# Kernel optimization log

Hardware: AMD Instinct MI355X
Metric: run time of the kernel (lower is better)

## Reference

```python
import jax, jax.numpy as jnp
import numpy as np

N = 100000   # input nodes
M = 100000   # output nodes (size = (N, M))
NNZ = 3_200_000  # edges, avg_degree 32
B = 32       # batch
D = 32       # Kaiming channel dim


def setup_inputs() -> dict:
    key = jax.random.key(0)
    k1, k2, k3 = jax.random.split(key, 3)
    # COO indices: row 0 = src (in [0, N)), row 1 = dst (in [0, M))
    indices = jax.random.randint(k1, (2, NNZ), 0, N, dtype=jnp.int32)
    # Kaiming init: randn * sqrt(2/d), as in the torch module when d is given
    values = jax.random.normal(k2, (NNZ,), dtype=jnp.float32) * np.float32((2.0 / D) ** 0.5)
    bias = jnp.zeros((M, 1), dtype=jnp.float32)
    x = jax.random.normal(k3, (B, N, 1), dtype=jnp.float32)
    return {"x": x, "indices": indices, "values": values, "bias": bias}


def reference(x, indices, values, bias):
    # Equivalent of: for each b, sparse.mm(W.T, x[b]) + bias, W in COO (N, M)
    # y[b, m] = sum_{e: dst[e]==m} values[e] * x[b, src[e]] + bias[m]
    src = indices[0]
    dst = indices[1]
    contrib = x[:, src, 0] * values[None, :]           # (B, NNZ) gather-multiply
    y = jax.ops.segment_sum(contrib.T, dst, num_segments=M)  # (M, B) scatter-add
    return (y.T + bias[:, 0][None, :])[..., None]       # (B, M, 1)
```

## Files before the change

### kernel.cpp

```cpp
#include <hip/hip_runtime.h>
#include <hip/hip_fp16.h>
#include <stdint.h>

#define NB 32
#define CSHIFT 7
#define CROWS 128
#define NC_MAX 1024
#define FCHUNK 8192
#define FTHREADS 1024
#define EPT (FCHUNK / FTHREADS)
#define CAP_C 4608
#define GTHREADS 512
#define NGW 8
#define GEPT ((CAP_C + GTHREADS - 1) / GTHREADS)
#define SRC_BITS 18
#define SRC_MASK ((1u << SRC_BITS) - 1)


__global__ void transpose_x_kernel(const float* __restrict__ x,
                                   __half* __restrict__ xt,
                                   int* __restrict__ zeroRegion, int N) {
    __shared__ float tile[32][33];
    if (blockIdx.x == 0) {
        int i = threadIdx.y * 32 + threadIdx.x;
        for (; i < NC_MAX + 4; i += 256) zeroRegion[i] = 0;
    }
    int n0 = blockIdx.x * 32;
    for (int i = threadIdx.y; i < 32; i += 8) {
        int n = n0 + threadIdx.x;
        tile[i][threadIdx.x] = (n < N) ? x[(size_t)i * N + n] : 0.f;
    }
    __syncthreads();
    for (int i = threadIdx.y; i < 32; i += 8) {
        int n = n0 + i;
        if (n < N) xt[(size_t)n * NB + threadIdx.x] =
            __float2half(tile[threadIdx.x][i]);
    }
}

__global__ __launch_bounds__(1024) void fill_coarse(
        const int* __restrict__ src,
        const int* __restrict__ dst,
        const float* __restrict__ vals,
        int* __restrict__ cCursor,
        uint2* __restrict__ csr,
        int* __restrict__ ovCount,
        int* __restrict__ ovList,
        int nnz) {
    __shared__ uint2 stage[FCHUNK];
    __shared__ unsigned short binOf[FCHUNK];
    __shared__ int lhist[NC_MAX];
    __shared__ int lbase[NC_MAX];
    __shared__ int delta[NC_MAX];
    int t = threadIdx.x;
    int e0 = blockIdx.x * FCHUNK;
    int chunk = min(FCHUNK, nnz - e0);
    int dcache[EPT], scache[EPT];
    float vcache[EPT];
    lhist[t] = 0;
    __syncthreads();
#pragma unroll
    for (int q = 0; q < EPT; ++q) {
        int e = e0 + q * FTHREADS + t;
        if (e < nnz) {
            int d = dst[e];
            dcache[q] = d;
            scache[q] = src[e];
            vcache[q] = vals[e];
            atomicAdd(&lhist[d >> CSHIFT], 1);
        } else dcache[q] = -1;
    }
    __syncthreads();
    int v = lhist[t];
    lbase[t] = v;
    __syncthreads();
    for (int off = 1; off < NC_MAX; off <<= 1) {
        int add = (t >= off) ? lbase[t - off] : 0;
        __syncthreads();
        lbase[t] += add;
        __syncthreads();
    }
    {
        int excl = lbase[t] - v;
        lbase[t] = excl;
        int grel = v ? atomicAdd(&cCursor[t], v) : 0;
        delta[t] = grel - excl;
        lhist[t] = 0;
    }
    __syncthreads();
#pragma unroll
    for (int q = 0; q < EPT; ++q) {
        int d = dcache[q];
        if (d >= 0) {
            int bin = d >> CSHIFT;
            int r = atomicAdd(&lhist[bin], 1);
            int pos = lbase[bin] + r;
            if (delta[bin] + pos < CAP_C) {
                stage[pos] = make_uint2(
                    ((uint32_t)(d & (CROWS - 1)) << SRC_BITS) |
                        (uint32_t)scache[q],
                    __float_as_uint(vcache[q]));
                binOf[pos] = (unsigned short)bin;
            } else {
                binOf[pos] = 0xFFFF;
                int op = atomicAdd(ovCount, 1);
                ovList[op] = e0 + q * FTHREADS + t;
            }
        }
    }
    __syncthreads();
    for (int idx = t; idx < chunk; idx += FTHREADS) {
        unsigned short bo = binOf[idx];
        if (bo != 0xFFFF)
            csr[(size_t)bo * CAP_C + delta[bo] + idx] = stage[idx];
    }
}

__global__ __launch_bounds__(GTHREADS) void region_sort_gather(
        const int* __restrict__ cCursor,
        const uint2* __restrict__ cCsr,
        const __half* __restrict__ xt,
        const float* __restrict__ bias,
        float* __restrict__ out, int M) {
    __shared__ uint2 sorted[CAP_C];
    __shared__ int whist[NGW][CROWS];
    __shared__ int rowOff[CROWS];
    __shared__ int rowCnt[CROWS];
    int c = blockIdx.x;
    int n = min(cCursor[c], CAP_C);
    int t = threadIdx.x;
    int w = t >> 6;
    uint2 ec[GEPT];
    for (int i = t; i < NGW * CROWS; i += GTHREADS) (&whist[0][0])[i] = 0;
    __syncthreads();
    const uint2* reg = cCsr + (size_t)c * CAP_C;
#pragma unroll
    for (int q = 0; q < GEPT; ++q) {
        int j = q * GTHREADS + t;
        if (j < n) {
            uint2 e = reg[j];
            ec[q] = e;
            atomicAdd(&whist[w][(e.x >> SRC_BITS) & (CROWS - 1)], 1);
        }
    }
    __syncthreads();
    int tot = 0;
    if (t < CROWS) {
#pragma unroll
        for (int w2 = 0; w2 < NGW; ++w2) tot += whist[w2][t];
        rowCnt[t] = tot;
        rowOff[t] = tot;
    }
    __syncthreads();
    for (int off = 1; off < CROWS; off <<= 1) {
        int add = (t < CROWS && t >= off) ? rowOff[t - off] : 0;
        __syncthreads();
        if (t < CROWS) rowOff[t] += add;
        __syncthreads();
    }
    if (t < CROWS) {
        int excl = rowOff[t] - rowCnt[t];
        rowOff[t] = excl;
        int run = excl;
#pragma unroll
        for (int w2 = 0; w2 < NGW; ++w2) {
            int cn = whist[w2][t];
            whist[w2][t] = run;
            run += cn;
        }
    }
    __syncthreads();
#pragma unroll
    for (int q = 0; q < GEPT; ++q) {
        int j = q * GTHREADS + t;
        if (j < n) {
            uint2 e = ec[q];
            int p = atomicAdd(&whist[w][(e.x >> SRC_BITS) & (CROWS - 1)], 1);
            sorted[p] = e;
        }
    }
    __syncthreads();
    int g = t >> 5;
    int b = t & 31;
    for (int r = g; r < CROWS; r += GTHREADS / 32) {
        int m = c * CROWS + r;
        if (m >= M) break;
        int jj   = rowOff[r];
        int jend = jj + rowCnt[r];
        float acc0 = 0.f, acc1 = 0.f;
        for (; jj + 8 <= jend; jj += 8) {
            uint2 e0 = sorted[jj + 0];
            uint2 e1 = sorted[jj + 1];
            uint2 e2 = sorted[jj + 2];
            uint2 e3 = sorted[jj + 3];
            uint2 e4 = sorted[jj + 4];
            uint2 e5 = sorted[jj + 5];
            uint2 e6 = sorted[jj + 6];
            uint2 e7 = sorted[jj + 7];
            float x0 = __half2float(xt[(size_t)(e0.x & SRC_MASK) * NB + b]);
            float x1 = __half2float(xt[(size_t)(e1.x & SRC_MASK) * NB + b]);
            float x2 = __half2float(xt[(size_t)(e2.x & SRC_MASK) * NB + b]);
            float x3 = __half2float(xt[(size_t)(e3.x & SRC_MASK) * NB + b]);
            float x4 = __half2float(xt[(size_t)(e4.x & SRC_MASK) * NB + b]);
            float x5 = __half2float(xt[(size_t)(e5.x & SRC_MASK) * NB + b]);
            float x6 = __half2float(xt[(size_t)(e6.x & SRC_MASK) * NB + b]);
            float x7 = __half2float(xt[(size_t)(e7.x & SRC_MASK) * NB + b]);
            acc0 = fmaf(__uint_as_float(e0.y), x0, acc0);
            acc1 = fmaf(__uint_as_float(e1.y), x1, acc1);
            acc0 = fmaf(__uint_as_float(e2.y), x2, acc0);
            acc1 = fmaf(__uint_as_float(e3.y), x3, acc1);
            acc0 = fmaf(__uint_as_float(e4.y), x4, acc0);
            acc1 = fmaf(__uint_as_float(e5.y), x5, acc1);
            acc0 = fmaf(__uint_as_float(e6.y), x6, acc0);
            acc1 = fmaf(__uint_as_float(e7.y), x7, acc1);
        }
        for (; jj < jend; ++jj) {
            uint2 e = sorted[jj];
            acc0 = fmaf(__uint_as_float(e.y),
                        __half2float(xt[(size_t)(e.x & SRC_MASK) * NB + b]),
                        acc0);
        }
        out[(size_t)b * M + m] = acc0 + acc1 + bias[m];
    }
}

__global__ void fixup_kernel(const int* __restrict__ ovCount,
                             const int* __restrict__ ovList,
                             const int* __restrict__ src,
                             const int* __restrict__ dst,
                             const float* __restrict__ vals,
                             const __half* __restrict__ xt,
                             float* __restrict__ out, int M) {
    long long total = (long long)(*ovCount) * 32;
    long long stride = (long long)gridDim.x * blockDim.x;
    for (long long i = (long long)blockIdx.x * blockDim.x + threadIdx.x;
         i < total; i += stride) {
        int k = (int)(i >> 5);
        int b = (int)(i & 31);
        int e = ovList[k];
        atomicAdd(&out[(size_t)b * M + dst[e]],
                  vals[e] * __half2float(xt[(size_t)src[e] * NB + b]));
    }
}

__global__ void finalize_kernel(const float* __restrict__ yt,
                                const float* __restrict__ bias,
                                float* __restrict__ out, int M) {
    __shared__ float tile[32][33];
    int m0 = blockIdx.x * 32;
    for (int i = threadIdx.y; i < 32; i += 8) {
        int m = m0 + i;
        tile[i][threadIdx.x] = (m < M) ? yt[(size_t)m * NB + threadIdx.x] : 0.f;
    }
    __syncthreads();
    for (int i = threadIdx.y; i < 32; i += 8) {
        int m = m0 + threadIdx.x;
        if (m < M) out[(size_t)i * M + m] = tile[threadIdx.x][i] + bias[m];
    }
}

__global__ void scatter_kernel(const int* __restrict__ src,
                               const int* __restrict__ dst,
                               const float* __restrict__ vals,
                               const __half* __restrict__ xt,
                               float* __restrict__ yt, int nnz) {
    long long tid = (long long)blockIdx.x * blockDim.x + threadIdx.x;
    int e = (int)(tid >> 5);
    if (e >= nnz) return;
    int b = (int)(tid & 31);
    atomicAdd(&yt[(size_t)dst[e] * NB + b],
              vals[e] * __half2float(xt[(size_t)src[e] * NB + b]));
}

extern "C" void kernel_launch(void* const* d_in, const int* in_sizes, int n_in,
                              void* d_out, int out_size, void* d_ws, size_t ws_size,
                              hipStream_t stream) {
    const float* x       = (const float*)d_in[0];
    const int*   indices = (const int*)  d_in[1];
    const float* vals    = (const float*)d_in[2];
    const float* bias    = (const float*)d_in[3];

    float* out = (float*)d_out;

    int nnz = in_sizes[1] / 2;
    int N   = in_sizes[0] / NB;
    int M   = in_sizes[3];

    const int* src = indices;
    const int* dst = indices + nnz;

    int ncoarse = (M + CROWS - 1) >> CSHIFT;

    __half* xt      = (__half*)d_ws;
    int*    cCursor = (int*)(xt + (size_t)N * NB);
    int*    ovCount = cCursor + NC_MAX;
    int*    ovList  = ovCount + 4;
    uint2*  cCsr    = (uint2*)(((uintptr_t)(ovList + nnz) + 15) &
                               ~(uintptr_t)15);

    size_t need = (size_t)((char*)(cCsr + (size_t)ncoarse * CAP_C) -
                           (char*)d_ws);

    float* yt = (float*)(xt + (size_t)N * NB);
    size_t need_fb = (size_t)((char*)(yt + (size_t)M * NB) - (char*)d_ws);

    if (ws_size >= need && ncoarse <= NC_MAX) {
        transpose_x_kernel<<<(N + 31) / 32, dim3(32, 8), 0, stream>>>(
            x, xt, cCursor, N);
        int fgrid = (nnz + FCHUNK - 1) / FCHUNK;
        fill_coarse<<<fgrid, FTHREADS, 0, stream>>>(src, dst, vals, cCursor,
                                                    cCsr, ovCount, ovList,
                                                    nnz);
        region_sort_gather<<<ncoarse, GTHREADS, 0, stream>>>(cCursor, cCsr,
                                                             xt, bias, out, M);
        fixup_kernel<<<32, 256, 0, stream>>>(ovCount, ovList, src, dst, vals,
                                             xt, out, M);
    } else if (ws_size >= need_fb) {
        transpose_x_kernel<<<(N + 31) / 32, dim3(32, 8), 0, stream>>>(
            x, xt, cCursor, N);
        hipMemsetAsync(yt, 0, (size_t)M * NB * sizeof(float), stream);
        long long pairs = (long long)nnz * NB;
        int grid = (int)((pairs + 255) / 256);
        scatter_kernel<<<grid, 256, 0, stream>>>(src, dst, vals, xt, yt, nnz);
        finalize_kernel<<<(M + 31) / 32, dim3(32, 8), 0, stream>>>(yt, bias,
                                                                   out, M);
    }
}
```

Baseline: 194.3 us.

## Halve shared memory staging in fill and gather kernels to raise occupancy

The fill kernel now runs 512 threads and stages the scattered edges in two passes through a 4096-entry shared buffer instead of one 8192-entry buffer. Each thread keeps the packed edge, bin and position in registers between passes. The gather kernel sorts and processes each 128-row region as two 64-row halves through a smaller shared buffer, with a slow rescan-from-global fallback when a half overflows. The aim is lower LDS use per block so more blocks fit per CU, paid for with extra barriers, more passes over the register caches and a rarely taken slow path.

```diff
diff --git a/kernel.cpp b/kernel.cpp
--- a/kernel.cpp
+++ b/kernel.cpp
@@ -7,12 +7,14 @@
 #define CROWS 128
 #define NC_MAX 1024
 #define FCHUNK 8192
-#define FTHREADS 1024
+#define FTHREADS 512
 #define EPT (FCHUNK / FTHREADS)
+#define HSTAGE 4096
 #define CAP_C 4608
 #define GTHREADS 512
 #define NGW 8
 #define GEPT ((CAP_C + GTHREADS - 1) / GTHREADS)
+#define HCAP 2816
 #define SRC_BITS 18
 #define SRC_MASK ((1u << SRC_BITS) - 1)
 
@@ -38,7 +40,7 @@
     }
 }
 
-__global__ __launch_bounds__(1024) void fill_coarse(
+__global__ __launch_bounds__(FTHREADS) void fill_coarse(
         const int* __restrict__ src,
         const int* __restrict__ dst,
         const float* __restrict__ vals,
@@ -47,72 +49,96 @@
         int* __restrict__ ovCount,
         int* __restrict__ ovList,
         int nnz) {
-    __shared__ uint2 stage[FCHUNK];
-    __shared__ unsigned short binOf[FCHUNK];
+    __shared__ uint2 stage[HSTAGE];
+    __shared__ unsigned short sbin[HSTAGE];
     __shared__ int lhist[NC_MAX];
     __shared__ int lbase[NC_MAX];
     __shared__ int delta[NC_MAX];
     int t = threadIdx.x;
     int e0 = blockIdx.x * FCHUNK;
     int chunk = min(FCHUNK, nnz - e0);
-    int dcache[EPT], scache[EPT];
-    float vcache[EPT];
-    lhist[t] = 0;
+    int      bcache[EPT];
+    uint32_t mcache[EPT];
+    uint32_t vcache[EPT];
+    int      pcache[EPT];
+    for (int i = t; i < NC_MAX; i += FTHREADS) lhist[i] = 0;
     __syncthreads();
 #pragma unroll
     for (int q = 0; q < EPT; ++q) {
         int e = e0 + q * FTHREADS + t;
         if (e < nnz) {
             int d = dst[e];
-            dcache[q] = d;
-            scache[q] = src[e];
-            vcache[q] = vals[e];
-            atomicAdd(&lhist[d >> CSHIFT], 1);
-        } else dcache[q] = -1;
-    }
-    __syncthreads();
-    int v = lhist[t];
-    lbase[t] = v;
-    __syncthreads();
-    for (int off = 1; off < NC_MAX; off <<= 1) {
+            int bin = d >> CSHIFT;
+            bcache[q] = bin;
+            mcache[q] = ((uint32_t)(d & (CROWS - 1)) << SRC_BITS) |
+                        (uint32_t)src[e];
+            vcache[q] = __float_as_uint(vals[e]);
+            atomicAdd(&lhist[bin], 1);
+        } else bcache[q] = -1;
+    }
+    __syncthreads();
+    int s0 = lhist[2 * t];
+    int s1 = lhist[2 * t + 1];
+    int tsum = s0 + s1;
+    lbase[t] = tsum;
+    __syncthreads();
+    for (int off = 1; off < FTHREADS; off <<= 1) {
         int add = (t >= off) ? lbase[t - off] : 0;
         __syncthreads();
         lbase[t] += add;
         __syncthreads();
     }
+    int texcl = lbase[t] - tsum;
+    __syncthreads();
+    lbase[2 * t]     = texcl;
+    lbase[2 * t + 1] = texcl + s0;
     {
-        int excl = lbase[t] - v;
-        lbase[t] = excl;
-        int grel = v ? atomicAdd(&cCursor[t], v) : 0;
-        delta[t] = grel - excl;
-        lhist[t] = 0;
+        int g0 = s0 ? atomicAdd(&cCursor[2 * t], s0) : 0;
+        int g1 = s1 ? atomicAdd(&cCursor[2 * t + 1], s1) : 0;
+        delta[2 * t]     = g0 - texcl;
+        delta[2 * t + 1] = g1 - (texcl + s0);
+        lhist[2 * t]     = 0;
+        lhist[2 * t + 1] = 0;
     }
     __syncthreads();
 #pragma unroll
     for (int q = 0; q < EPT; ++q) {
-        int d = dcache[q];
-        if (d >= 0) {
-            int bin = d >> CSHIFT;
+        int bin = bcache[q];
+        if (bin >= 0) {
             int r = atomicAdd(&lhist[bin], 1);
             int pos = lbase[bin] + r;
-            if (delta[bin] + pos < CAP_C) {
-                stage[pos] = make_uint2(
-                    ((uint32_t)(d & (CROWS - 1)) << SRC_BITS) |
-                        (uint32_t)scache[q],
-                    __float_as_uint(vcache[q]));
-                binOf[pos] = (unsigned short)bin;
-            } else {
-                binOf[pos] = 0xFFFF;
+            pcache[q] = pos;
+            if (delta[bin] + pos >= CAP_C) {
+                bcache[q] = -2;
                 int op = atomicAdd(ovCount, 1);
                 ovList[op] = e0 + q * FTHREADS + t;
             }
         }
     }
     __syncthreads();
-    for (int idx = t; idx < chunk; idx += FTHREADS) {
-        unsigned short bo = binOf[idx];
-        if (bo != 0xFFFF)
-            csr[(size_t)bo * CAP_C + delta[bo] + idx] = stage[idx];
+    for (int h = 0; h < FCHUNK / HSTAGE; ++h) {
+        int lo = h * HSTAGE;
+#pragma unroll
+        for (int q = 0; q < EPT; ++q) {
+            if (bcache[q] != -1) {
+                int p = pcache[q];
+                if (p >= lo && p < lo + HSTAGE) {
+                    int s = p - lo;
+                    if (bcache[q] >= 0) {
+                        stage[s] = make_uint2(mcache[q], vcache[q]);
+                        sbin[s] = (unsigned short)bcache[q];
+                    } else sbin[s] = 0xFFFF;
+                }
+            }
+        }
+        __syncthreads();
+        int lim = min(HSTAGE, chunk - lo);
+        for (int idx = t; idx < lim; idx += FTHREADS) {
+            unsigned short bo = sbin[idx];
+            if (bo != 0xFFFF)
+                csr[(size_t)bo * CAP_C + delta[bo] + lo + idx] = stage[idx];
+        }
+        __syncthreads();
     }
 }
 
@@ -122,10 +148,11 @@
         const __half* __restrict__ xt,
         const float* __restrict__ bias,
         float* __restrict__ out, int M) {
-    __shared__ uint2 sorted[CAP_C];
+    __shared__ uint2 sorted[HCAP];
     __shared__ int whist[NGW][CROWS];
     __shared__ int rowOff[CROWS];
     __shared__ int rowCnt[CROWS];
+    __shared__ int halfBase;
     int c = blockIdx.x;
     int n = min(cCursor[c], CAP_C);
     int t = threadIdx.x;
@@ -161,6 +188,7 @@
     if (t < CROWS) {
         int excl = rowOff[t] - rowCnt[t];
         rowOff[t] = excl;
+        if (t == 64) halfBase = excl;
         int run = excl;
 #pragma unroll
         for (int w2 = 0; w2 < NGW; ++w2) {
@@ -170,57 +198,82 @@
         }
     }
     __syncthreads();
-#pragma unroll
-    for (int q = 0; q < GEPT; ++q) {
-        int j = q * GTHREADS + t;
-        if (j < n) {
-            uint2 e = ec[q];
-            int p = atomicAdd(&whist[w][(e.x >> SRC_BITS) & (CROWS - 1)], 1);
-            sorted[p] = e;
-        }
-    }
-    __syncthreads();
     int g = t >> 5;
     int b = t & 31;
-    for (int r = g; r < CROWS; r += GTHREADS / 32) {
-        int m = c * CROWS + r;
-        if (m >= M) break;
-        int jj   = rowOff[r];
-        int jend = jj + rowCnt[r];
-        float acc0 = 0.f, acc1 = 0.f;
-        for (; jj + 8 <= jend; jj += 8) {
-            uint2 e0 = sorted[jj + 0];
-            uint2 e1 = sorted[jj + 1];
-            uint2 e2 = sorted[jj + 2];
-            uint2 e3 = sorted[jj + 3];
-            uint2 e4 = sorted[jj + 4];
-            uint2 e5 = sorted[jj + 5];
-            uint2 e6 = sorted[jj + 6];
-            uint2 e7 = sorted[jj + 7];
-            float x0 = __half2float(xt[(size_t)(e0.x & SRC_MASK) * NB + b]);
-            float x1 = __half2float(xt[(size_t)(e1.x & SRC_MASK) * NB + b]);
-            float x2 = __half2float(xt[(size_t)(e2.x & SRC_MASK) * NB + b]);
-            float x3 = __half2float(xt[(size_t)(e3.x & SRC_MASK) * NB + b]);
-            float x4 = __half2float(xt[(size_t)(e4.x & SRC_MASK) * NB + b]);
-            float x5 = __half2float(xt[(size_t)(e5.x & SRC_MASK) * NB + b]);
-            float x6 = __half2float(xt[(size_t)(e6.x & SRC_MASK) * NB + b]);
-            float x7 = __half2float(xt[(size_t)(e7.x & SRC_MASK) * NB + b]);
-            acc0 = fmaf(__uint_as_float(e0.y), x0, acc0);
-            acc1 = fmaf(__uint_as_float(e1.y), x1, acc1);
-            acc0 = fmaf(__uint_as_float(e2.y), x2, acc0);
-            acc1 = fmaf(__uint_as_float(e3.y), x3, acc1);
-            acc0 = fmaf(__uint_as_float(e4.y), x4, acc0);
-            acc1 = fmaf(__uint_as_float(e5.y), x5, acc1);
-            acc0 = fmaf(__uint_as_float(e6.y), x6, acc0);
-            acc1 = fmaf(__uint_as_float(e7.y), x7, acc1);
-        }
-        for (; jj < jend; ++jj) {
-            uint2 e = sorted[jj];
-            acc0 = fmaf(__uint_as_float(e.y),
-                        __half2float(xt[(size_t)(e.x & SRC_MASK) * NB + b]),
-                        acc0);
-        }
-        out[(size_t)b * M + m] = acc0 + acc1 + bias[m];
+    int half0 = halfBase;
+    int half1 = n - halfBase;
+
+    if (half0 <= HCAP && half1 <= HCAP) {
+        for (int h = 0; h < 2; ++h) {
+            int hb = h ? halfBase : 0;
+#pragma unroll
+            for (int q = 0; q < GEPT; ++q) {
+                int j = q * GTHREADS + t;
+                if (j < n) {
+                    int row = (ec[q].x >> SRC_BITS) & (CROWS - 1);
+                    if ((row >> 6) == h) {
+                        int p = atomicAdd(&whist[w][row], 1) - hb;
+                        sorted[p] = ec[q];
+                    }
+                }
+            }
+            __syncthreads();
+            for (int r = (h << 6) + g; r < (h << 6) + 64; r += 16) {
+                int m = c * CROWS + r;
+                if (m >= M) continue;
+                int jj   = rowOff[r] - hb;
+                int jend = jj + rowCnt[r];
+                float acc0 = 0.f, acc1 = 0.f;
+                for (; jj + 8 <= jend; jj += 8) {
+                    uint2 e0 = sorted[jj + 0];
+                    uint2 e1 = sorted[jj + 1];
+                    uint2 e2 = sorted[jj + 2];
+                    uint2 e3 = sorted[jj + 3];
+                    uint2 e4 = sorted[jj + 4];
+                    uint2 e5 = sorted[jj + 5];
+                    uint2 e6 = sorted[jj + 6];
+                    uint2 e7 = sorted[jj + 7];
+                    float x0 = __half2float(xt[(size_t)(e0.x & SRC_MASK) * NB + b]);
+                    float x1 = __half2float(xt[(size_t)(e1.x & SRC_MASK) * NB + b]);
+                    float x2 = __half2float(xt[(size_t)(e2.x & SRC_MASK) * NB + b]);
+                    float x3 = __half2float(xt[(size_t)(e3.x & SRC_MASK) * NB + b]);
+                    float x4 = __half2float(xt[(size_t)(e4.x & SRC_MASK) * NB + b]);
+                    float x5 = __half2float(xt[(size_t)(e5.x & SRC_MASK) * NB + b]);
+                    float x6 = __half2float(xt[(size_t)(e6.x & SRC_MASK) * NB + b]);
+                    float x7 = __half2float(xt[(size_t)(e7.x & SRC_MASK) * NB + b]);
+                    acc0 = fmaf(__uint_as_float(e0.y), x0, acc0);
+                    acc1 = fmaf(__uint_as_float(e1.y), x1, acc1);
+                    acc0 = fmaf(__uint_as_float(e2.y), x2, acc0);
+                    acc1 = fmaf(__uint_as_float(e3.y), x3, acc1);
+                    acc0 = fmaf(__uint_as_float(e4.y), x4, acc0);
+                    acc1 = fmaf(__uint_as_float(e5.y), x5, acc1);
+                    acc0 = fmaf(__uint_as_float(e6.y), x6, acc0);
+                    acc1 = fmaf(__uint_as_float(e7.y), x7, acc1);
+                }
+                for (; jj < jend; ++jj) {
+                    uint2 e = sorted[jj];
+                    acc0 = fmaf(__uint_as_float(e.y),
+                                __half2float(xt[(size_t)(e.x & SRC_MASK) * NB + b]),
+                                acc0);
+                }
+                out[(size_t)b * M + m] = acc0 + acc1 + bias[m];
+            }
+            __syncthreads();
+        }
+    } else {
+        for (int r = g; r < CROWS; r += 16) {
+            int m = c * CROWS + r;
+            if (m >= M) continue;
+            float acc = 0.f;
+            for (int j = 0; j < n; ++j) {
+                uint2 e = reg[j];
+                if ((int)((e.x >> SRC_BITS) & (CROWS - 1)) == r)
+                    acc = fmaf(__uint_as_float(e.y),
+                               __half2float(xt[(size_t)(e.x & SRC_MASK) * NB + b]),
+                               acc);
+            }
+            out[(size_t)b * M + m] = acc + bias[m];
+        }
     }
 }
 
```

Result: faster. 176.8 us (-9.0%).
